# Performance work log

Measured on AMD Instinct MI355X. Metric: run time of the kernel, lower is better.

Reference implementation:

```python
import jax, jax.numpy as jnp
import numpy as np

B, S, HID, NH = 2, 2048, 2048, 16
HD = HID // NH  # head_dim = 128


def setup_inputs() -> dict:
    key = jax.random.key(0)
    ks = jax.random.split(key, 10)
    sc = 1.0 / np.sqrt(HID)
    inp = {
        "hidden_state": jax.random.normal(ks[0], (B, S, HID), dtype=jnp.float32),
        # upper-triangular (strict) causal mask: 1 where attention is forbidden
        "casual_mask": jnp.triu(jnp.ones((S, S), dtype=jnp.float32), k=1),
        # pad last 128 tokens of each sequence
        "pad_mask": jnp.concatenate(
            [jnp.zeros((B, S - 128), jnp.float32), jnp.ones((B, 128), jnp.float32)], axis=1
        ),
        # weights stored [in, out] (transposed vs torch Linear)
        "Wq": jax.random.normal(ks[1], (HID, HID), dtype=jnp.float32) * sc,
        "bq": jnp.zeros((HID,), jnp.float32),
        "Wk": jax.random.normal(ks[2], (HID, HD), dtype=jnp.float32) * sc,
        "bk": jnp.zeros((HD,), jnp.float32),
        "Wv": jax.random.normal(ks[3], (HID, HD), dtype=jnp.float32) * sc,
        "bv": jnp.zeros((HD,), jnp.float32),
        "Wo": jax.random.normal(ks[4], (HID, HID), dtype=jnp.float32) * sc,
        "bo": jnp.zeros((HID,), jnp.float32),
    }
    return inp


def reference(hidden_state, casual_mask, pad_mask, Wq, bq, Wk, bk, Wv, bv, Wo, bo):
    bsz, seq_len, hid = hidden_state.shape
    nh = NH
    hd = hid // nh
    q = hidden_state @ Wq + bq                      # [B,S,HID]
    k = hidden_state @ Wk + bk                      # [B,S,HD]  single shared head
    v = hidden_state @ Wv + bv                      # [B,S,HD]
    q = q.reshape(bsz, seq_len, nh, hd).transpose(0, 2, 1, 3)  # [B,NH,S,HD]
    # attn scores: shared K broadcast across all query heads
    scores = jnp.einsum("bhqd,bkd->bhqk", q, k) / jnp.sqrt(jnp.float32(hd))
    scores = scores + casual_mask * (-1e9)
    scores = scores + pad_mask[:, None, None, :] * (-1e9)
    probs = jax.nn.softmax(scores, axis=-1)         # [B,NH,S,S]
    out = jnp.einsum("bhqk,bkd->bhqd", probs, v)    # [B,NH,S,HD]
    out = out.transpose(0, 2, 1, 3).reshape(bsz, seq_len, hid)
    return out @ Wo + bo
```

## Files before the change

kernel.cpp:

```cpp
#include <hip/hip_runtime.h>
#include <hip/hip_bf16.h>
#include <math.h>

#define B_    2
#define S_    2048
#define HID_  2048
#define NH_   16
#define HD_   128
#define MTOT  4096
#define QKV_N 2304

typedef short bf16x8 __attribute__((ext_vector_type(8)));
typedef float f32x4  __attribute__((ext_vector_type(4)));
typedef float f32x16 __attribute__((ext_vector_type(16)));

__device__ __forceinline__ ushort f2bf(float f) {
    __hip_bfloat16 h = __float2bfloat16(f);
    ushort u; __builtin_memcpy(&u, &h, 2); return u;
}

__device__ __forceinline__ uint cvtpk_bf16(float lo, float hi) {
    uint r;
    asm("v_cvt_pk_bf16_f32 %0, %1, %2" : "=v"(r) : "v"(lo), "v"(hi));
    return r;
}

__device__ __forceinline__ void gload_lds16(const void* g, void* l) {
    __builtin_amdgcn_global_load_lds(
        (const __attribute__((address_space(1))) void*)g,
        (__attribute__((address_space(3))) void*)l, 16, 0, 0);
}

__global__ void prep(const float* __restrict__ hidden, ushort* __restrict__ hbf,
                     const float* __restrict__ Wq, const float* __restrict__ Wk,
                     const float* __restrict__ Wv, const float* __restrict__ Wo,
                     ushort* __restrict__ WqkvT, ushort* __restrict__ WoT,
                     const float* __restrict__ bq, const float* __restrict__ bk,
                     const float* __restrict__ bv, float* __restrict__ bqkv,
                     int* __restrict__ ctr)
{
    __shared__ float tile[32][33];
    const int bid = blockIdx.x;
    const int tid = threadIdx.x;

    if (bid < 4096) {
        long i = ((long)bid * 256 + tid) * 8;
        float4 a = *(const float4*)&hidden[i];
        float4 b = *(const float4*)&hidden[i + 4];
        uint4 o;
        o.x = (uint)f2bf(a.x) | ((uint)f2bf(a.y) << 16);
        o.y = (uint)f2bf(a.z) | ((uint)f2bf(a.w) << 16);
        o.z = (uint)f2bf(b.x) | ((uint)f2bf(b.y) << 16);
        o.w = (uint)f2bf(b.z) | ((uint)f2bf(b.w) << 16);
        *(uint4*)&hbf[i] = o;
        return;
    }
    if (bid >= 12800) {
        int i = (bid - 12800) * 256 + tid;
        if (i == 0) *ctr = 0;
        if (i < 2048)      bqkv[i] = bq[i];
        else if (i < 2176) bqkv[i] = bk[i - 2048];
        else if (i < QKV_N) bqkv[i] = bv[i - 2176];
        return;
    }

    const float* W; ushort* T; int N, rowoff, r;
    if (bid < 8192)      { W = Wq; T = WqkvT; N = 2048; rowoff = 0;    r = bid - 4096; }
    else if (bid < 8448) { W = Wk; T = WqkvT; N = 128;  rowoff = 2048; r = bid - 8192; }
    else if (bid < 8704) { W = Wv; T = WqkvT; N = 128;  rowoff = 2176; r = bid - 8448; }
    else                 { W = Wo; T = WoT;   N = 2048; rowoff = 0;    r = bid - 8704; }
    const int nxt = N >> 5;
    const int bx = r % nxt, by = r / nxt;
    const int tx = tid & 31, ty = tid >> 5;
    const int n0 = bx * 32, k0 = by * 32;
#pragma unroll
    for (int i = 0; i < 4; i++)
        tile[ty + 8 * i][tx] = W[(long)(k0 + ty + 8 * i) * N + n0 + tx];
    __syncthreads();
#pragma unroll
    for (int i = 0; i < 4; i++)
        T[(long)(rowoff + n0 + ty + 8 * i) * 2048 + k0 + tx] = f2bf(tile[tx][ty + 8 * i]);
}

__global__ __launch_bounds__(256, 3) void gemm_qkv(
    const ushort* __restrict__ A, const ushort* __restrict__ Bt,
    const float* __restrict__ bias,
    ushort* __restrict__ qbuf, ushort* __restrict__ kbuf,
    ushort* __restrict__ vtbuf)
{
    const int K = HID_;
    __shared__ __align__(16) ushort As[2 * 128 * 32];
    __shared__ __align__(16) ushort Bs[2 * 128 * 32];
    const int t = threadIdx.x;
    const int w = t >> 6, l = t & 63;
    const long bm = (long)blockIdx.y * 128;
    const long bn = (long)blockIdx.x * 128;

    f32x4 acc[4][4];
#pragma unroll
    for (int i = 0; i < 4; i++)
#pragma unroll
        for (int j = 0; j < 4; j++) acc[i][j] = (f32x4){0.f, 0.f, 0.f, 0.f};

    const int srow = w * 16 + (l >> 2);
    const int scol = (l & 3) * 8;
    const ushort* Ag0 = A + (bm + srow) * (long)K + scol;
    const ushort* Ag1 = A + (bm + srow + 64) * (long)K + scol;
    const ushort* Bg0 = Bt + (bn + srow) * (long)K + scol;
    const ushort* Bg1 = Bt + (bn + srow + 64) * (long)K + scol;
    ushort* Al0 = As + w * 512;
    ushort* Al1 = As + 2048 + w * 512;
    ushort* Bl0 = Bs + w * 512;
    ushort* Bl1 = Bs + 2048 + w * 512;

    const int mrow = l & 15, kq = l >> 4;
    const int moff = (w & 1) * 64, noff = (w >> 1) * 64;

    gload_lds16(Ag0, Al0);
    gload_lds16(Ag1, Al1);
    gload_lds16(Bg0, Bl0);
    gload_lds16(Bg1, Bl1);
    __syncthreads();

    for (int k0 = 0; k0 < K; k0 += 32) {
        const int cb = (k0 >> 5) & 1;
        const int po = cb * 4096;
        if (k0 + 32 < K) {
            const int pn = (cb ^ 1) * 4096;
            gload_lds16(Ag0 + k0 + 32, Al0 + pn);
            gload_lds16(Ag1 + k0 + 32, Al1 + pn);
            gload_lds16(Bg0 + k0 + 32, Bl0 + pn);
            gload_lds16(Bg1 + k0 + 32, Bl1 + pn);
        }
        bf16x8 af[4], bfr[4];
#pragma unroll
        for (int i = 0; i < 4; i++)
            af[i] = *(const bf16x8*)&As[po + (moff + i * 16 + mrow) * 32 + kq * 8];
#pragma unroll
        for (int j = 0; j < 4; j++)
            bfr[j] = *(const bf16x8*)&Bs[po + (noff + j * 16 + mrow) * 32 + kq * 8];
#pragma unroll
        for (int i = 0; i < 4; i++)
#pragma unroll
            for (int j = 0; j < 4; j++)
                acc[i][j] = __builtin_amdgcn_mfma_f32_16x16x32_bf16(
                    af[i], bfr[j], acc[i][j], 0, 0, 0);
        __syncthreads();
    }

    const int crow = (l >> 4) * 4, ccol = l & 15;
    const int tile = blockIdx.x;
#pragma unroll
    for (int i = 0; i < 4; i++) {
#pragma unroll
        for (int j = 0; j < 4; j++) {
            long colg = bn + noff + j * 16 + ccol;
            float bv = bias[colg];
            long row0 = bm + moff + i * 16 + crow;
            float v[4];
#pragma unroll
            for (int r = 0; r < 4; r++) v[r] = acc[i][j][r] + bv;
            if (tile < 16) {
#pragma unroll
                for (int r = 0; r < 4; r++)
                    qbuf[(row0 + r) * (long)HID_ + colg] = f2bf(v[r]);
            } else if (tile == 16) {
                long ck = colg - 2048;
#pragma unroll
                for (int r = 0; r < 4; r++)
                    kbuf[(row0 + r) * (long)HD_ + ck] = f2bf(v[r]);
            } else {
                long cv = colg - 2176;
                long b  = row0 >> 11;
                long s0 = row0 & 2047;
                ushort4 pk;
                pk.x = f2bf(v[0]); pk.y = f2bf(v[1]);
                pk.z = f2bf(v[2]); pk.w = f2bf(v[3]);
                *(ushort4*)&vtbuf[b * (HD_ * (long)S_) + cv * (long)S_ + s0] = pk;
            }
        }
    }
}

__global__ __launch_bounds__(256, 3) void gemm_mfma(
    const ushort* __restrict__ A, const ushort* __restrict__ Bt,
    const float* __restrict__ bias, float* __restrict__ C,
    int K, int ldc)
{
    __shared__ __align__(16) ushort As[2 * 128 * 32];
    __shared__ __align__(16) ushort Bs[2 * 128 * 32];
    const int t = threadIdx.x;
    const int w = t >> 6, l = t & 63;
    const long bm = (long)blockIdx.y * 128;
    const long bn = (long)blockIdx.x * 128;

    f32x4 acc[4][4];
#pragma unroll
    for (int i = 0; i < 4; i++)
#pragma unroll
        for (int j = 0; j < 4; j++) acc[i][j] = (f32x4){0.f, 0.f, 0.f, 0.f};

    const int srow = w * 16 + (l >> 2);
    const int scol = (l & 3) * 8;
    const ushort* Ag0 = A + (bm + srow) * (long)K + scol;
    const ushort* Ag1 = A + (bm + srow + 64) * (long)K + scol;
    const ushort* Bg0 = Bt + (bn + srow) * (long)K + scol;
    const ushort* Bg1 = Bt + (bn + srow + 64) * (long)K + scol;
    ushort* Al0 = As + w * 512;
    ushort* Al1 = As + 2048 + w * 512;
    ushort* Bl0 = Bs + w * 512;
    ushort* Bl1 = Bs + 2048 + w * 512;

    const int mrow = l & 15, kq = l >> 4;
    const int moff = (w & 1) * 64, noff = (w >> 1) * 64;

    gload_lds16(Ag0, Al0);
    gload_lds16(Ag1, Al1);
    gload_lds16(Bg0, Bl0);
    gload_lds16(Bg1, Bl1);
    __syncthreads();

    for (int k0 = 0; k0 < K; k0 += 32) {
        const int cb = (k0 >> 5) & 1;
        const int po = cb * 4096;
        if (k0 + 32 < K) {
            const int pn = (cb ^ 1) * 4096;
            gload_lds16(Ag0 + k0 + 32, Al0 + pn);
            gload_lds16(Ag1 + k0 + 32, Al1 + pn);
            gload_lds16(Bg0 + k0 + 32, Bl0 + pn);
            gload_lds16(Bg1 + k0 + 32, Bl1 + pn);
        }
        bf16x8 af[4], bfr[4];
#pragma unroll
        for (int i = 0; i < 4; i++)
            af[i] = *(const bf16x8*)&As[po + (moff + i * 16 + mrow) * 32 + kq * 8];
#pragma unroll
        for (int j = 0; j < 4; j++)
            bfr[j] = *(const bf16x8*)&Bs[po + (noff + j * 16 + mrow) * 32 + kq * 8];
#pragma unroll
        for (int i = 0; i < 4; i++)
#pragma unroll
            for (int j = 0; j < 4; j++)
                acc[i][j] = __builtin_amdgcn_mfma_f32_16x16x32_bf16(
                    af[i], bfr[j], acc[i][j], 0, 0, 0);
        __syncthreads();
    }

    const int crow = (l >> 4) * 4, ccol = l & 15;
#pragma unroll
    for (int i = 0; i < 4; i++) {
#pragma unroll
        for (int j = 0; j < 4; j++) {
            long col = bn + noff + j * 16 + ccol;
            float bv = bias[col];
#pragma unroll
            for (int r = 0; r < 4; r++) {
                long row = bm + moff + i * 16 + crow + r;
                C[row * (long)ldc + col] = acc[i][j][r] + bv;
            }
        }
    }
}

__global__ __launch_bounds__(512, 1) void attn_mfma(
    const ushort* __restrict__ qbuf, const ushort* __restrict__ kbuf,
    const ushort* __restrict__ vtbuf, ushort* __restrict__ outp,
    int* __restrict__ workctr)
{
    __shared__ __align__(16) char smem[86016];
    ushort* KsB = (ushort*)smem;
    ushort* VtB = (ushort*)(smem + 32768);
    float*  OP  = (float*)smem;
    float*  LP  = (float*)(smem + 65536);
    int*    sidx = (int*)(smem + 66048);

    const int t = threadIdx.x, w = t >> 6, l = t & 63;
    const int wq = w & 3, kh = w >> 2;
    const int l31 = l & 31, h5 = l >> 5;

    int koff[2], klo[2], voff[2], vlo[2];
#pragma unroll
    for (int i = 0; i < 2; i++) {
        const int c = w * 2 + i;
        const int key0 = c * 4 + (l >> 4);
        const int gk = (l & 15) ^ (key0 & 15);
        koff[i] = key0 * HD_ + gk * 8;
        klo[i]  = c * 512 + l * 8;
        const int d = c * 8 + (l >> 3);
        const int gv = (l & 7) ^ (d & 7);
        voff[i] = d * S_ + gv * 8;
        vlo[i]  = c * 512 + l * 8;
    }

    const float SC = 0.08838834764831845f * 1.44269504089f;

    for (;;) {
        if (t == 0) *sidx = atomicAdd(workctr, 1);
        __syncthreads();
        const int idx = *sidx;
        if (idx >= 512) break;

        const int qblk = 15 - (idx >> 5);
        const int hb = idx & 31;
        const int h = hb & 15, b = hb >> 4;
        const long rowbase = (long)b * S_;
        const int qbase = qblk * 128 + wq * 32;
        const int qmaxw = qbase + 31;
        const int kTiles = 2 * qblk + 2;
        const ushort* kb0 = kbuf + rowbase * (long)HD_;
        const ushort* vb0 = vtbuf + (long)b * (HD_ * (long)S_);

        bf16x8 qf[8];
        {
            const ushort* qp = qbuf + (rowbase + qbase + l31) * (long)HID_
                                    + h * HD_ + h5 * 8;
#pragma unroll
            for (int ks = 0; ks < 8; ks++) qf[ks] = *(const bf16x8*)(qp + ks * 16);
        }

        f32x16 o[4] = {};
        float lrun = 0.f;

#pragma unroll
        for (int i = 0; i < 2; i++) {
            gload_lds16(kb0 + koff[i], KsB + klo[i]);
            gload_lds16(vb0 + voff[i], VtB + vlo[i]);
        }
        __syncthreads();

        for (int kt = 0; kt < kTiles; kt++) {
            const int cur = kt & 1;
            const int ktb = kt * 64;

            if (kt + 1 < kTiles) {
                const int nxt = cur ^ 1;
                const int nb = ktb + 64;
#pragma unroll
                for (int i = 0; i < 2; i++) {
                    gload_lds16(kb0 + koff[i] + (long)nb * HD_,
                                KsB + nxt * 8192 + klo[i]);
                    gload_lds16(vb0 + voff[i] + nb, VtB + nxt * 8192 + vlo[i]);
                }
            }

            if (ktb <= qmaxw) {
                const ushort* Ks = KsB + cur * 8192;
                const ushort* Vt = VtB + cur * 8192;

                f32x16 c0 = {};
                const int key = kh * 32 + l31;
#pragma unroll
                for (int ks = 0; ks < 8; ks++) {
                    const int g = (ks * 2 + h5) ^ (key & 15);
                    bf16x8 a = *(const bf16x8*)&Ks[key * 128 + g * 8];
                    c0 = __builtin_amdgcn_mfma_f32_32x32x16_bf16(
                        a, qf[ks], c0, 0, 0, 0);
                }

                const bool boundary = (ktb + 63 > qbase) || (ktb >= S_ - 128);
                if (boundary) {
                    const int qg = qbase + l31;
#pragma unroll
                    for (int g = 0; g < 4; g++)
#pragma unroll
                        for (int r = 0; r < 4; r++) {
                            const int keyg = ktb + kh * 32 + 4 * h5 + 8 * g + r;
                            if (keyg > qg || keyg >= S_ - 128)
                                c0[g * 4 + r] = -3.0e38f;
                        }
                }

                float s0 = 0.f, s1 = 0.f, s2 = 0.f, s3 = 0.f;
#pragma unroll
                for (int g = 0; g < 4; g++) {
                    float p0 = __builtin_amdgcn_exp2f(c0[g * 4 + 0] * SC);
                    float p1 = __builtin_amdgcn_exp2f(c0[g * 4 + 1] * SC);
                    float p2 = __builtin_amdgcn_exp2f(c0[g * 4 + 2] * SC);
                    float p3 = __builtin_amdgcn_exp2f(c0[g * 4 + 3] * SC);
                    c0[g * 4 + 0] = p0; s0 += p0;
                    c0[g * 4 + 1] = p1; s1 += p1;
                    c0[g * 4 + 2] = p2; s2 += p2;
                    c0[g * 4 + 3] = p3; s3 += p3;
                }
                float sum = (s0 + s1) + (s2 + s3);
                sum += __shfl_xor(sum, 32);
                lrun += sum;

#pragma unroll
                for (int j = 0; j < 2; j++) {
                    const int base = j * 8;
                    uint X  = cvtpk_bf16(c0[base + 0], c0[base + 1]);
                    uint Y  = cvtpk_bf16(c0[base + 2], c0[base + 3]);
                    uint Z  = cvtpk_bf16(c0[base + 4], c0[base + 5]);
                    uint Wd = cvtpk_bf16(c0[base + 6], c0[base + 7]);
                    asm("v_permlane32_swap_b32 %0, %1" : "+v"(X), "+v"(Z));
                    asm("v_permlane32_swap_b32 %0, %1" : "+v"(Y), "+v"(Wd));
                    uint tmp[4] = {X, Y, Z, Wd};
                    bf16x8 pf;
                    __builtin_memcpy(&pf, tmp, 16);
                    const int ks2 = kh * 2 + j;
#pragma unroll
                    for (int mb = 0; mb < 4; mb++) {
                        const int d = mb * 32 + l31;
                        const int g = (ks2 * 2 + h5) ^ (d & 7);
                        bf16x8 a = *(const bf16x8*)&Vt[d * 64 + g * 8];
                        o[mb] = __builtin_amdgcn_mfma_f32_32x32x16_bf16(
                            a, pf, o[mb], 0, 0, 0);
                    }
                }
            }
            __syncthreads();
        }

        if (kh == 1) {
#pragma unroll
            for (int mb = 0; mb < 4; mb++)
#pragma unroll
                for (int r = 0; r < 16; r++) {
                    const int d = mb * 32 + (r & 3) + 8 * (r >> 2) + 4 * h5;
                    OP[wq * 4096 + d * 32 + l31] = o[mb][r];
                }
            LP[wq * 32 + l31] = lrun;
        }
        __syncthreads();
        if (kh == 0) {
#pragma unroll
            for (int mb = 0; mb < 4; mb++)
#pragma unroll
                for (int r = 0; r < 16; r++) {
                    const int d = mb * 32 + (r & 3) + 8 * (r >> 2) + 4 * h5;
                    o[mb][r] += OP[wq * 4096 + d * 32 + l31];
                }
            lrun += LP[wq * 32 + l31];
        }
        __syncthreads();

        if (kh == 0) {
            ushort* Ob = (ushort*)smem + wq * 4352;
            const float inv = 1.f / lrun;
#pragma unroll
            for (int mb = 0; mb < 4; mb++) {
#pragma unroll
                for (int g = 0; g < 4; g++) {
                    const int d0 = mb * 32 + 4 * h5 + 8 * g;
                    ushort4 pk;
                    pk.x = f2bf(o[mb][g * 4 + 0] * inv);
                    pk.y = f2bf(o[mb][g * 4 + 1] * inv);
                    pk.z = f2bf(o[mb][g * 4 + 2] * inv);
                    pk.w = f2bf(o[mb][g * 4 + 3] * inv);
                    *(ushort4*)&Ob[l31 * 136 + d0] = pk;
                }
            }
            __builtin_amdgcn_s_waitcnt(0);
            const int q = l >> 1, half = l & 1;
            const ushort* src = Ob + q * 136 + half * 64;
            ushort* dst = outp + (rowbase + qblk * 128 + wq * 32 + q) * (long)HID_
                               + h * HD_ + half * 64;
#pragma unroll
            for (int i = 0; i < 8; i++) {
                uint4 v = *(const uint4*)(src + i * 8);
                *(uint4*)(dst + i * 8) = v;
            }
        }
    }
}

extern "C" void kernel_launch(void* const* d_in, const int* in_sizes, int n_in,
                              void* d_out, int out_size, void* d_ws, size_t ws_size,
                              hipStream_t stream)
{
    const float* hidden = (const float*)d_in[0];
    const float* Wq  = (const float*)d_in[3];
    const float* bq  = (const float*)d_in[4];
    const float* Wk  = (const float*)d_in[5];
    const float* bk  = (const float*)d_in[6];
    const float* Wv  = (const float*)d_in[7];
    const float* bv  = (const float*)d_in[8];
    const float* Wo  = (const float*)d_in[9];
    const float* bo  = (const float*)d_in[10];
    float* out = (float*)d_out;

    char* ws = (char*)d_ws;
    ushort* hbf   = (ushort*)(ws);
    ushort* WqkvT = (ushort*)(ws + 16777216);
    ushort* WoT   = (ushort*)(ws + 26214400);
    float*  bqkv  = (float*) (ws + 34603008);
    int*    wctr  = (int*)   (ws + 34612224);
    ushort* qbuf  = (ushort*)(ws + 34619392);
    ushort* kbuf  = (ushort*)(ws + 51396608);
    ushort* vtbuf = (ushort*)(ws + 52445184);
    ushort* attnO = (ushort*)(ws + 53493760);

    prep<<<12809, 256, 0, stream>>>(hidden, hbf, Wq, Wk, Wv, Wo,
                                    WqkvT, WoT, bq, bk, bv, bqkv, wctr);
    gemm_qkv<<<dim3(18, 32), 256, 0, stream>>>(hbf, WqkvT, bqkv,
                                               qbuf, kbuf, vtbuf);
    attn_mfma<<<256, 512, 0, stream>>>(qbuf, kbuf, vtbuf, attnO, wctr);
    gemm_mfma<<<dim3(16, 32), 256, 0, stream>>>(attnO, WoT, bo, out,
                                                HID_, HID_);
}
```

Baseline: 284.0 us.

## Double attention key tile to 128 and skip fully padded final tile

The attention kernel now processes 128 keys per tile instead of 64, so each wave computes two 32-key score blocks per iteration and the K/V shared-memory buffers double to 64 KB each. The goal is to halve the number of loop iterations, barriers and prefetch rounds. The tile count is also capped at 15, which skips the last 128-key tile because those keys are all padding and fully masked. The cost is higher LDS use (about 128 KB) and more registers per wave, and the V swizzle now uses 16 groups instead of 8.

```diff
diff --git a/kernel.cpp b/kernel.cpp
--- a/kernel.cpp
+++ b/kernel.cpp
@@ -267,27 +267,27 @@
     const ushort* __restrict__ vtbuf, ushort* __restrict__ outp,
     int* __restrict__ workctr)
 {
-    __shared__ __align__(16) char smem[86016];
+    __shared__ __align__(16) char smem[131648];
     ushort* KsB = (ushort*)smem;
-    ushort* VtB = (ushort*)(smem + 32768);
+    ushort* VtB = (ushort*)(smem + 65536);
     float*  OP  = (float*)smem;
-    float*  LP  = (float*)(smem + 65536);
-    int*    sidx = (int*)(smem + 66048);
+    int*    sidx = (int*)(smem + 131072);
+    float*  LP  = (float*)(smem + 131088);
 
     const int t = threadIdx.x, w = t >> 6, l = t & 63;
     const int wq = w & 3, kh = w >> 2;
     const int l31 = l & 31, h5 = l >> 5;
 
-    int koff[2], klo[2], voff[2], vlo[2];
-#pragma unroll
-    for (int i = 0; i < 2; i++) {
-        const int c = w * 2 + i;
+    int koff[4], klo[4], voff[4], vlo[4];
+#pragma unroll
+    for (int i = 0; i < 4; i++) {
+        const int c = w * 4 + i;
         const int key0 = c * 4 + (l >> 4);
         const int gk = (l & 15) ^ (key0 & 15);
         koff[i] = key0 * HD_ + gk * 8;
         klo[i]  = c * 512 + l * 8;
-        const int d = c * 8 + (l >> 3);
-        const int gv = (l & 7) ^ (d & 7);
+        const int d = c * 4 + (l >> 4);
+        const int gv = (l & 15) ^ (d & 15);
         voff[i] = d * S_ + gv * 8;
         vlo[i]  = c * 512 + l * 8;
     }
@@ -306,7 +306,7 @@
         const long rowbase = (long)b * S_;
         const int qbase = qblk * 128 + wq * 32;
         const int qmaxw = qbase + 31;
-        const int kTiles = 2 * qblk + 2;
+        const int kTiles = (qblk + 1 < 15) ? (qblk + 1) : 15;
         const ushort* kb0 = kbuf + rowbase * (long)HD_;
         const ushort* vb0 = vtbuf + (long)b * (HD_ * (long)S_);
 
@@ -322,7 +322,7 @@
         float lrun = 0.f;
 
 #pragma unroll
-        for (int i = 0; i < 2; i++) {
+        for (int i = 0; i < 4; i++) {
             gload_lds16(kb0 + koff[i], KsB + klo[i]);
             gload_lds16(vb0 + voff[i], VtB + vlo[i]);
         }
@@ -330,80 +330,89 @@
 
         for (int kt = 0; kt < kTiles; kt++) {
             const int cur = kt & 1;
-            const int ktb = kt * 64;
+            const int ktb = kt * 128;
 
             if (kt + 1 < kTiles) {
                 const int nxt = cur ^ 1;
-                const int nb = ktb + 64;
-#pragma unroll
-                for (int i = 0; i < 2; i++) {
-                    gload_lds16(kb0 + koff[i] + (long)nb * HD_,
-                                KsB + nxt * 8192 + klo[i]);
-                    gload_lds16(vb0 + voff[i] + nb, VtB + nxt * 8192 + vlo[i]);
+                const long nb = (long)(ktb + 128);
+#pragma unroll
+                for (int i = 0; i < 4; i++) {
+                    gload_lds16(kb0 + koff[i] + nb * HD_,
+                                KsB + nxt * 16384 + klo[i]);
+                    gload_lds16(vb0 + voff[i] + nb, VtB + nxt * 16384 + vlo[i]);
                 }
             }
 
             if (ktb <= qmaxw) {
-                const ushort* Ks = KsB + cur * 8192;
-                const ushort* Vt = VtB + cur * 8192;
-
-                f32x16 c0 = {};
-                const int key = kh * 32 + l31;
-#pragma unroll
-                for (int ks = 0; ks < 8; ks++) {
-                    const int g = (ks * 2 + h5) ^ (key & 15);
-                    bf16x8 a = *(const bf16x8*)&Ks[key * 128 + g * 8];
-                    c0 = __builtin_amdgcn_mfma_f32_32x32x16_bf16(
-                        a, qf[ks], c0, 0, 0, 0);
-                }
-
-                const bool boundary = (ktb + 63 > qbase) || (ktb >= S_ - 128);
+                const ushort* Ks = KsB + cur * 16384;
+                const ushort* Vt = VtB + cur * 16384;
+
+                f32x16 c[2] = {};
+#pragma unroll
+                for (int mb = 0; mb < 2; mb++) {
+                    const int key = kh * 64 + mb * 32 + l31;
+#pragma unroll
+                    for (int ks = 0; ks < 8; ks++) {
+                        const int g = (ks * 2 + h5) ^ (key & 15);
+                        bf16x8 a = *(const bf16x8*)&Ks[key * 128 + g * 8];
+                        c[mb] = __builtin_amdgcn_mfma_f32_32x32x16_bf16(
+                            a, qf[ks], c[mb], 0, 0, 0);
+                    }
+                }
+
+                const bool boundary = (ktb + 127 > qbase) || (ktb + 127 >= S_ - 128);
                 if (boundary) {
                     const int qg = qbase + l31;
 #pragma unroll
-                    for (int g = 0; g < 4; g++)
-#pragma unroll
-                        for (int r = 0; r < 4; r++) {
-                            const int keyg = ktb + kh * 32 + 4 * h5 + 8 * g + r;
-                            if (keyg > qg || keyg >= S_ - 128)
-                                c0[g * 4 + r] = -3.0e38f;
-                        }
+                    for (int mb = 0; mb < 2; mb++)
+#pragma unroll
+                        for (int g = 0; g < 4; g++)
+#pragma unroll
+                            for (int r = 0; r < 4; r++) {
+                                const int keyg = ktb + kh * 64 + mb * 32
+                                               + 4 * h5 + 8 * g + r;
+                                if (keyg > qg || keyg >= S_ - 128)
+                                    c[mb][g * 4 + r] = -3.0e38f;
+                            }
                 }
 
                 float s0 = 0.f, s1 = 0.f, s2 = 0.f, s3 = 0.f;
 #pragma unroll
-                for (int g = 0; g < 4; g++) {
-                    float p0 = __builtin_amdgcn_exp2f(c0[g * 4 + 0] * SC);
-                    float p1 = __builtin_amdgcn_exp2f(c0[g * 4 + 1] * SC);
-                    float p2 = __builtin_amdgcn_exp2f(c0[g * 4 + 2] * SC);
-                    float p3 = __builtin_amdgcn_exp2f(c0[g * 4 + 3] * SC);
-                    c0[g * 4 + 0] = p0; s0 += p0;
-                    c0[g * 4 + 1] = p1; s1 += p1;
-                    c0[g * 4 + 2] = p2; s2 += p2;
-                    c0[g * 4 + 3] = p3; s3 += p3;
-                }
+                for (int mb = 0; mb < 2; mb++)
+#pragma unroll
+                    for (int g = 0; g < 4; g++) {
+                        float p0 = __builtin_amdgcn_exp2f(c[mb][g * 4 + 0] * SC);
+                        float p1 = __builtin_amdgcn_exp2f(c[mb][g * 4 + 1] * SC);
+                        float p2 = __builtin_amdgcn_exp2f(c[mb][g * 4 + 2] * SC);
+                        float p3 = __builtin_amdgcn_exp2f(c[mb][g * 4 + 3] * SC);
+                        c[mb][g * 4 + 0] = p0; s0 += p0;
+                        c[mb][g * 4 + 1] = p1; s1 += p1;
+                        c[mb][g * 4 + 2] = p2; s2 += p2;
+                        c[mb][g * 4 + 3] = p3; s3 += p3;
+                    }
                 float sum = (s0 + s1) + (s2 + s3);
                 sum += __shfl_xor(sum, 32);
                 lrun += sum;
 
 #pragma unroll
-                for (int j = 0; j < 2; j++) {
-                    const int base = j * 8;
-                    uint X  = cvtpk_bf16(c0[base + 0], c0[base + 1]);
-                    uint Y  = cvtpk_bf16(c0[base + 2], c0[base + 3]);
-                    uint Z  = cvtpk_bf16(c0[base + 4], c0[base + 5]);
-                    uint Wd = cvtpk_bf16(c0[base + 6], c0[base + 7]);
+                for (int k2 = 0; k2 < 4; k2++) {
+                    const int mbs = k2 >> 1;
+                    const int base = (k2 & 1) * 8;
+                    uint X  = cvtpk_bf16(c[mbs][base + 0], c[mbs][base + 1]);
+                    uint Y  = cvtpk_bf16(c[mbs][base + 2], c[mbs][base + 3]);
+                    uint Z  = cvtpk_bf16(c[mbs][base + 4], c[mbs][base + 5]);
+                    uint Wd = cvtpk_bf16(c[mbs][base + 6], c[mbs][base + 7]);
                     asm("v_permlane32_swap_b32 %0, %1" : "+v"(X), "+v"(Z));
                     asm("v_permlane32_swap_b32 %0, %1" : "+v"(Y), "+v"(Wd));
                     uint tmp[4] = {X, Y, Z, Wd};
                     bf16x8 pf;
                     __builtin_memcpy(&pf, tmp, 16);
-                    const int ks2 = kh * 2 + j;
+                    const int ks2 = kh * 4 + k2;
 #pragma unroll
                     for (int mb = 0; mb < 4; mb++) {
                         const int d = mb * 32 + l31;
-                        const int g = (ks2 * 2 + h5) ^ (d & 7);
-                        bf16x8 a = *(const bf16x8*)&Vt[d * 64 + g * 8];
+                        const int g = (ks2 * 2 + h5) ^ (d & 15);
+                        bf16x8 a = *(const bf16x8*)&Vt[d * 128 + g * 8];
                         o[mb] = __builtin_amdgcn_mfma_f32_32x32x16_bf16(
                             a, pf, o[mb], 0, 0, 0);
                     }
```

New measurement: 284.7 us. No clear change (+0.2%).
